# Kernel optimization log

Measured on AMD Instinct MI355X. Metric: run time of the kernel, lower is better.

## Reference

```python
import jax, jax.numpy as jnp
import numpy as np

B, CIN, H, W = 16, 32, 256, 256
COUT, KH, KW = 32, 3, 3
NUM_EXPERTS = 8
PAD = ((1, 1), (1, 1))  # static 'same' padding for 3x3, stride 1, dilation 1


def setup_inputs() -> dict:
    key = jax.random.key(0)
    k_x, k_r, k_w, k_b = jax.random.split(key, 4)
    x = jax.random.normal(k_x, (B, CIN, H, W), dtype=jnp.float32)
    # routing weights are typically sigmoid/softmax outputs in [0,1]
    routing_weights = jax.nn.softmax(jax.random.normal(k_r, (B, NUM_EXPERTS), dtype=jnp.float32), axis=-1)
    num_params = COUT * CIN * KH * KW  # groups=1 -> in_channels//groups = CIN
    expert_weight = jax.random.normal(k_w, (NUM_EXPERTS, num_params), dtype=jnp.float32) * 0.05
    expert_bias = jax.random.normal(k_b, (NUM_EXPERTS, COUT), dtype=jnp.float32) * 0.05
    return {"x": x, "routing_weights": routing_weights,
            "expert_weight": expert_weight, "expert_bias": expert_bias}


def reference(x, routing_weights, expert_weight, expert_bias):
    b = x.shape[0]
    # Per-sample kernels: [B, num_params] -> [B, COUT, CIN, KH, KW]
    w = jnp.matmul(routing_weights, expert_weight).reshape(b, COUT, CIN, KH, KW)
    bias = jnp.matmul(routing_weights, expert_bias)  # [B, COUT]

    def conv_one(xi, wi):
        # xi: [CIN, H, W], wi: [COUT, CIN, KH, KW]
        return jax.lax.conv_general_dilated(
            xi[None], wi, window_strides=(1, 1), padding=PAD,
            dimension_numbers=("NCHW", "OIHW", "NCHW"))[0]

    out = jax.vmap(conv_one)(x, w)  # [B, COUT, H, W]
    out = out + bias[:, :, None, None]
    return out
```

## Files before the change

### kernel.cpp

```cpp
#include <hip/hip_runtime.h>

#define B_   16
#define CIN  32
#define COUT 32
#define HH   256
#define WW   256
#define NE   8
#define NTAP 9
#define KTOT (NTAP * CIN)

#define TH 8
#define TW 64
#define LROWS (TH + 2)
#define LCOLS (TW + 2)
#define PXS   40

typedef __attribute__((ext_vector_type(8))) short  short8;
typedef __attribute__((ext_vector_type(4))) float  floatx4;

__device__ __forceinline__ unsigned short f2bf(float f) {
    unsigned int u = __float_as_uint(f);
    u += 0x7FFFu + ((u >> 16) & 1u);
    return (unsigned short)(u >> 16);
}

__global__ __launch_bounds__(256) void prep_weights(
    const float* __restrict__ routing,
    const float* __restrict__ ew,
    const float* __restrict__ eb,
    unsigned short* __restrict__ ws_w,
    float* __restrict__ ws_b)
{
    const int b = blockIdx.x;
    const int t = threadIdx.x;
    float r[NE];
#pragma unroll
    for (int e = 0; e < NE; ++e) r[e] = routing[b * NE + e];

    for (int idx = t; idx < COUT * KTOT; idx += 256) {
        const int co  = idx / KTOT;
        const int k   = idx - co * KTOT;
        const int tap = k >> 5;
        const int ci  = k & 31;
        float acc = 0.f;
#pragma unroll
        for (int e = 0; e < NE; ++e)
            acc += r[e] * ew[e * (COUT * CIN * 9) + co * (CIN * 9) + ci * 9 + tap];
        ws_w[(b * COUT + co) * KTOT + k] = f2bf(acc);
    }
    if (t < COUT) {
        float acc = 0.f;
#pragma unroll
        for (int e = 0; e < NE; ++e) acc += r[e] * eb[e * COUT + t];
        ws_b[b * COUT + t] = acc;
    }
}

__global__ __launch_bounds__(256) void condconv_mfma(
    const float* __restrict__ x,
    const unsigned short* __restrict__ wsw,
    const float* __restrict__ wsb,
    float* __restrict__ out)
{
    __shared__ __align__(16) unsigned short s_x[LROWS * LCOLS * PXS];

    const int b    = blockIdx.z;
    const int x0   = blockIdx.x * TW;
    const int y0   = blockIdx.y * TH;
    const int t    = threadIdx.x;
    const int lane = t & 63;
    const int wv   = t >> 6;
    const int ln   = lane & 15;
    const int quad = lane >> 4;

    short8 afrag[NTAP][2];
    {
        const unsigned short* wb = wsw + (size_t)b * COUT * KTOT;
#pragma unroll
        for (int tap = 0; tap < NTAP; ++tap)
#pragma unroll
            for (int h = 0; h < 2; ++h)
                afrag[tap][h] = *(const short8*)(wb + (h * 16 + ln) * KTOT + tap * 32 + quad * 8);
    }
    float bias_v[2][4];
#pragma unroll
    for (int h = 0; h < 2; ++h)
#pragma unroll
        for (int rg = 0; rg < 4; ++rg)
            bias_v[h][rg] = wsb[b * COUT + h * 16 + quad * 4 + rg];

    for (int task = t; task < LROWS * LCOLS * 4; task += 256) {
        const int p   = task >> 2;
        const int c   = task & 3;
        const int row = p / LCOLS;
        const int col = p - row * LCOLS;
        const int gy  = y0 + row - 1;
        const int gx  = x0 + col - 1;
        short8 pk;
        if (gy >= 0 && gy < HH && gx >= 0 && gx < WW) {
            const float* src = x + (((size_t)b * CIN + c * 8) * HH + gy) * WW + gx;
#pragma unroll
            for (int u = 0; u < 8; ++u)
                pk[u] = (short)f2bf(src[(size_t)u * HH * WW]);
        } else {
#pragma unroll
            for (int u = 0; u < 8; ++u) pk[u] = 0;
        }
        *(short8*)&s_x[p * PXS + c * 8] = pk;
    }
    __syncthreads();

    floatx4 acc[8][2];
#pragma unroll
    for (int tt = 0; tt < 8; ++tt)
#pragma unroll
        for (int h = 0; h < 2; ++h)
            acc[tt][h] = (floatx4){0.f, 0.f, 0.f, 0.f};

#pragma unroll
    for (int tap = 0; tap < NTAP; ++tap) {
        const int dy = tap / 3;
        const int dx = tap - dy * 3;
#pragma unroll
        for (int tt = 0; tt < 8; ++tt) {
            const int r    = 2 * wv + (tt >> 2);
            const int q    = tt & 3;
            const int lrow = r + dy;
            const int lcol = q * 16 + ln + dx;
            const short8 bfr = *(const short8*)&s_x[(lrow * LCOLS + lcol) * PXS + quad * 8];
            acc[tt][0] = __builtin_amdgcn_mfma_f32_16x16x32_bf16(afrag[tap][0], bfr, acc[tt][0], 0, 0, 0);
            acc[tt][1] = __builtin_amdgcn_mfma_f32_16x16x32_bf16(afrag[tap][1], bfr, acc[tt][1], 0, 0, 0);
        }
    }

#pragma unroll
    for (int tt = 0; tt < 8; ++tt) {
        const int r  = 2 * wv + (tt >> 2);
        const int q  = tt & 3;
        const int gy = y0 + r;
        const int gx = x0 + q * 16 + ln;
#pragma unroll
        for (int h = 0; h < 2; ++h)
#pragma unroll
            for (int rg = 0; rg < 4; ++rg) {
                const int co = h * 16 + quad * 4 + rg;
                out[(((size_t)b * COUT + co) * HH + gy) * WW + gx] = acc[tt][h][rg] + bias_v[h][rg];
            }
    }
}

extern "C" void kernel_launch(void* const* d_in, const int* in_sizes, int n_in,
                              void* d_out, int out_size, void* d_ws, size_t ws_size,
                              hipStream_t stream) {
    const float* x       = (const float*)d_in[0];
    const float* routing = (const float*)d_in[1];
    const float* ew      = (const float*)d_in[2];
    const float* eb      = (const float*)d_in[3];
    float* out = (float*)d_out;

    unsigned short* ws_w = (unsigned short*)d_ws;
    float* ws_b = (float*)((char*)d_ws + (size_t)B_ * COUT * KTOT * 2);

    prep_weights<<<dim3(B_), dim3(256), 0, stream>>>(routing, ew, eb, ws_w, ws_b);

    dim3 grid(WW / TW, HH / TH, B_);
    condconv_mfma<<<grid, dim3(256), 0, stream>>>(x, ws_w, ws_b, out);
}
```

Baseline: 274.2 us.

## Halve tile width, stream weight fragments per tap to cut registers

The conv tile width drops from 64 to 32 columns, so each wave holds four accumulator tiles instead of eight. The whole 9-tap weight fragment array is no longer held in registers. Each tap's fragment is now loaded from global memory one tap ahead inside a non-unrolled loop, and the bias load moves after the main loop. Launch bounds request 4 blocks per CU. The aim is lower register pressure and higher occupancy, at the cost of a larger halo fraction (34/32 vs 66/64 columns), more blocks, and repeated weight reads per block.

```diff
diff --git a/kernel.cpp b/kernel.cpp
--- a/kernel.cpp
+++ b/kernel.cpp
@@ -10,7 +10,7 @@
 #define KTOT (NTAP * CIN)
 
 #define TH 8
-#define TW 64
+#define TW 32
 #define LROWS (TH + 2)
 #define LCOLS (TW + 2)
 #define PXS   40
@@ -56,7 +56,7 @@
     }
 }
 
-__global__ __launch_bounds__(256) void condconv_mfma(
+__global__ __launch_bounds__(256, 4) void condconv_mfma(
     const float* __restrict__ x,
     const unsigned short* __restrict__ wsw,
     const float* __restrict__ wsb,
@@ -72,22 +72,6 @@
     const int wv   = t >> 6;
     const int ln   = lane & 15;
     const int quad = lane >> 4;
-
-    short8 afrag[NTAP][2];
-    {
-        const unsigned short* wb = wsw + (size_t)b * COUT * KTOT;
-#pragma unroll
-        for (int tap = 0; tap < NTAP; ++tap)
-#pragma unroll
-            for (int h = 0; h < 2; ++h)
-                afrag[tap][h] = *(const short8*)(wb + (h * 16 + ln) * KTOT + tap * 32 + quad * 8);
-    }
-    float bias_v[2][4];
-#pragma unroll
-    for (int h = 0; h < 2; ++h)
-#pragma unroll
-        for (int rg = 0; rg < 4; ++rg)
-            bias_v[h][rg] = wsb[b * COUT + h * 16 + quad * 4 + rg];
 
     for (int task = t; task < LROWS * LCOLS * 4; task += 256) {
         const int p   = task >> 2;
@@ -108,35 +92,54 @@
         }
         *(short8*)&s_x[p * PXS + c * 8] = pk;
     }
-    __syncthreads();
 
-    floatx4 acc[8][2];
+    const unsigned short* wb = wsw + (size_t)b * COUT * KTOT;
+    short8 afc0 = *(const short8*)(wb + ln * KTOT + quad * 8);
+    short8 afc1 = *(const short8*)(wb + (16 + ln) * KTOT + quad * 8);
+
+    floatx4 acc[4][2];
 #pragma unroll
-    for (int tt = 0; tt < 8; ++tt)
+    for (int tt = 0; tt < 4; ++tt)
 #pragma unroll
         for (int h = 0; h < 2; ++h)
             acc[tt][h] = (floatx4){0.f, 0.f, 0.f, 0.f};
 
+    int base[4];
 #pragma unroll
+    for (int tt = 0; tt < 4; ++tt)
+        base[tt] = ((2 * wv + (tt >> 1)) * LCOLS + (tt & 1) * 16 + ln) * PXS + quad * 8;
+
+    __syncthreads();
+
+#pragma unroll 1
     for (int tap = 0; tap < NTAP; ++tap) {
-        const int dy = tap / 3;
-        const int dx = tap - dy * 3;
+        const int tn = (tap < NTAP - 1) ? tap + 1 : NTAP - 1;
+        const short8 afn0 = *(const short8*)(wb + ln * KTOT + tn * 32 + quad * 8);
+        const short8 afn1 = *(const short8*)(wb + (16 + ln) * KTOT + tn * 32 + quad * 8);
+        const int dy  = tap / 3;
+        const int dx  = tap - dy * 3;
+        const int off = (dy * LCOLS + dx) * PXS;
 #pragma unroll
-        for (int tt = 0; tt < 8; ++tt) {
-            const int r    = 2 * wv + (tt >> 2);
-            const int q    = tt & 3;
-            const int lrow = r + dy;
-            const int lcol = q * 16 + ln + dx;
-            const short8 bfr = *(const short8*)&s_x[(lrow * LCOLS + lcol) * PXS + quad * 8];
-            acc[tt][0] = __builtin_amdgcn_mfma_f32_16x16x32_bf16(afrag[tap][0], bfr, acc[tt][0], 0, 0, 0);
-            acc[tt][1] = __builtin_amdgcn_mfma_f32_16x16x32_bf16(afrag[tap][1], bfr, acc[tt][1], 0, 0, 0);
+        for (int tt = 0; tt < 4; ++tt) {
+            const short8 bfr = *(const short8*)&s_x[base[tt] + off];
+            acc[tt][0] = __builtin_amdgcn_mfma_f32_16x16x32_bf16(afc0, bfr, acc[tt][0], 0, 0, 0);
+            acc[tt][1] = __builtin_amdgcn_mfma_f32_16x16x32_bf16(afc1, bfr, acc[tt][1], 0, 0, 0);
         }
+        afc0 = afn0;
+        afc1 = afn1;
     }
 
+    float bias_v[2][4];
 #pragma unroll
-    for (int tt = 0; tt < 8; ++tt) {
-        const int r  = 2 * wv + (tt >> 2);
-        const int q  = tt & 3;
+    for (int h = 0; h < 2; ++h)
+#pragma unroll
+        for (int rg = 0; rg < 4; ++rg)
+            bias_v[h][rg] = wsb[b * COUT + h * 16 + quad * 4 + rg];
+
+#pragma unroll
+    for (int tt = 0; tt < 4; ++tt) {
+        const int r  = 2 * wv + (tt >> 1);
+        const int q  = tt & 1;
         const int gy = y0 + r;
         const int gx = x0 + q * 16 + ln;
 #pragma unroll
```

New measurement: 299.4 us. +9.2%, slower.
